# Performance work log

Hardware: AMD Instinct MI355X
Metric: run time of the kernel (lower is better)

## Reference

```python
import jax, jax.numpy as jnp
import numpy as np

NUM_REL = 6
EMBED_DIM = 128
B, N = 8, 1024


def _relation_type(dx, dy):
    # Faithful to _get_relation_type's if/elif chain (order matters).
    return jnp.select(
        [dy > 0.5,
         dy < -0.5,
         dx < -0.5,
         dx > 0.5,
         (jnp.abs(dx) < 0.3) & (jnp.abs(dy) < 0.3)],
        [0, 1, 2, 3, 4],
        5,
    )


def setup_inputs() -> dict:
    key = jax.random.key(0)
    k1, k2, k3, k4 = jax.random.split(key, 4)
    symbols = jax.random.normal(k1, (B, N, EMBED_DIM), dtype=jnp.float32)
    positions = jax.random.normal(k2, (B, N, 2), dtype=jnp.float32)
    # 6 Linear(embed_dim, embed_dim) layers, stacked: W [6, D, D] (torch layout: y = x @ W.T + b)
    bound = 1.0 / np.sqrt(EMBED_DIM)
    W = jax.random.uniform(k3, (NUM_REL, EMBED_DIM, EMBED_DIM), dtype=jnp.float32,
                           minval=-bound, maxval=bound)
    b = jax.random.uniform(k4, (NUM_REL, EMBED_DIM), dtype=jnp.float32,
                           minval=-bound, maxval=bound)
    return {"symbols": symbols, "positions": positions, "W": W, "b": b}


def reference(symbols, positions, W, b):
    Bn, Nn, D = symbols.shape
    # dx[b,i,j] = pos[b,j,0] - pos[b,i,0]; dy likewise (source i -> target j)
    dx = positions[:, None, :, 0] - positions[:, :, None, 0]  # [B, i, j]
    dy = positions[:, None, :, 1] - positions[:, :, None, 1]
    rel = _relation_type(dx, dy)  # [B, i, j] in {0..5}

    # Per-type transform of every source symbol: T[r,b,i,:] = symbols[b,i] @ W[r].T + b[r]
    T = jnp.einsum('bid,red->rbie', symbols, W) + b[:, None, None, :]  # [6, B, N, D]

    # One-hot relation mask with i != j excluded; scatter-add into targets j.
    not_diag = ~jnp.eye(Nn, dtype=bool)  # [i, j]
    mask = (rel[None] == jnp.arange(NUM_REL)[:, None, None, None]) & not_diag  # [6, B, i, j]
    agg = jnp.einsum('rbij,rbie->bje', mask.astype(symbols.dtype), T)  # [B, N, D]
    return symbols + agg
```

## Files before the change

### kernel.cpp

```cpp
#include <hip/hip_runtime.h>
#include <stdint.h>


typedef __attribute__((ext_vector_type(8))) short bf16x8;
typedef __attribute__((ext_vector_type(4))) float f32x4;
union U4B { uint4 u; bf16x8 b; };

#if defined(__has_builtin)
#  if __has_builtin(__builtin_amdgcn_global_load_lds)
#    define HAVE_GLL 1
#  endif
#  if __has_builtin(__builtin_amdgcn_mul_u24)
#    define OH_MUL24 1
#  endif
#endif

__device__ __forceinline__ uint16_t f2bf(float f) {
    union { float f; uint32_t u; } v; v.f = f;
    uint32_t u = v.u;
    uint32_t r = (u + 0x7FFFu + ((u >> 16) & 1u)) >> 16;
    return (uint16_t)r;
}

#define BARRIER_LGKM() do {                                   \
    asm volatile("s_waitcnt lgkmcnt(0)" ::: "memory");        \
    __builtin_amdgcn_s_barrier();                             \
    asm volatile("" ::: "memory");                            \
} while (0)

__global__ __launch_bounds__(256)
void prep_kernel(const float* __restrict__ X, const float* __restrict__ W,
                 uint16_t* __restrict__ symT, uint16_t* __restrict__ WtB,
                 float* __restrict__ T4) {
    const int blk = blockIdx.x, tid = threadIdx.x;
    if (blk < 256) {
        __shared__ float T[64 * 65];
        const int b = blk & 7, z = blk >> 3, it = z & 15, et = z >> 4;
        const int i0 = it * 64, e0 = et * 64;
        const float4* Xf = (const float4*)X;
#pragma unroll
        for (int s = 0; s < 4; ++s) {
            int il = s * 16 + (tid >> 4), e4 = tid & 15;
            float4 v = Xf[((size_t)b << 15) + (size_t)((i0 + il) << 5) + (e0 >> 2) + e4];
            T[il * 65 + e4 * 4 + 0] = v.x;
            T[il * 65 + e4 * 4 + 1] = v.y;
            T[il * 65 + e4 * 4 + 2] = v.z;
            T[il * 65 + e4 * 4 + 3] = v.w;
        }
        __syncthreads();
#pragma unroll
        for (int s = 0; s < 4; ++s) {
            int el = s * 16 + (tid >> 4), il4 = tid & 15;
            uint16_t h0 = f2bf(T[(il4 * 4 + 0) * 65 + el]);
            uint16_t h1 = f2bf(T[(il4 * 4 + 1) * 65 + el]);
            uint16_t h2 = f2bf(T[(il4 * 4 + 2) * 65 + el]);
            uint16_t h3 = f2bf(T[(il4 * 4 + 3) * 65 + el]);
            uint2 pk = { (uint32_t)h0 | ((uint32_t)h1 << 16),
                         (uint32_t)h2 | ((uint32_t)h3 << 16) };
            *(uint2*)&symT[((size_t)b << 17) + ((size_t)(e0 + el) << 10) + i0 + il4 * 4] = pk;
        }
    } else if (blk < 352) {
        int g = (blk - 256) * 256 + tid;
        float4 v = ((const float4*)W)[g];
        int r = g >> 12, rem = g & 4095, ep = rem >> 5, e4 = rem & 31;
        int kb = r * 4 + (e4 >> 3);
        int kc = (e4 & 7) * 4;
        uint16_t h0 = f2bf(v.x), h1 = f2bf(v.y), h2 = f2bf(v.z), h3 = f2bf(v.w);
        uint2 pk = { (uint32_t)h0 | ((uint32_t)h1 << 16),
                     (uint32_t)h2 | ((uint32_t)h3 << 16) };
        *(uint2*)&WtB[((size_t)(kb * 128 + ep)) * 32 + kc] = pk;
    } else {
        const int z = blk - 352, bb = z >> 2, qq = z & 3;
        const int e = tid & 127, half = tid >> 7;
        const float* base = X + (((size_t)(bb << 10) + (qq << 8) + (half << 7)) << 7) + e;
        float s = 0.f;
#pragma unroll 8
        for (int itr = 0; itr < 128; ++itr) s += base[(size_t)itr << 7];
        __shared__ float red[256];
        red[tid] = s;
        __syncthreads();
        if (tid < 128) T4[(z << 7) + tid] = red[tid] + red[tid + 128];
    }
}

#define SP 776

__global__ __launch_bounds__(512, 8)
void fused_kernel(const float* __restrict__ X, const float* __restrict__ pos,
                  const uint16_t* __restrict__ symT, const uint16_t* __restrict__ WtB,
                  const float* __restrict__ bias, const float* __restrict__ T4,
                  float* __restrict__ out) {
    __shared__ __align__(16) char smem[40960];
    float2*   posS  = (float2*)(smem + 16384);
    uint16_t* SA    = (uint16_t*)smem;
    float*    cntL  = (float*)(smem + 24832);
    uint32_t* rel32 = (uint32_t*)(smem + 32768);

    const int blk = blockIdx.x;
    const int b = blk & 7, jt = blk >> 3, j0 = jt * 8;
    const int tid = threadIdx.x;
    const int w = tid >> 6, lane = tid & 63, m = lane & 15, q = lane >> 4;

    const uint16_t* symTb = symT + ((size_t)b << 17);

    int goff[2];
#pragma unroll
    for (int s = 0; s < 2; ++s) {
        int e = (w << 4) + (s << 3) + (lane >> 3);
        int t = lane & 7;
        goff[s] = (e << 10) + ((t ^ (e & 7)) << 3);
    }

    auto issue_chunk = [&](int cidx, int bufsel) {
#ifdef HAVE_GLL
#pragma unroll
        for (int s = 0; s < 2; ++s) {
            const uint16_t* gp = symTb + goff[s] + cidx * 64;
            char* lp = smem + bufsel * 16384 + (w << 11) + (s << 10);
            typedef const __attribute__((address_space(1))) uint32_t gu32;
            typedef __attribute__((address_space(3))) uint32_t lu32;
            __builtin_amdgcn_global_load_lds((gu32*)gp, (lu32*)lp, 16, 0, 0);
        }
#else
#pragma unroll
        for (int s = 0; s < 2; ++s) {
            uint4 v = *(const uint4*)(symTb + goff[s] + cidx * 64);
            *(uint4*)(smem + bufsel * 16384 + (w << 11) + (s << 10) + lane * 16) = v;
        }
#endif
    };

    issue_chunk(0, 0);
    const float2* pos2 = (const float2*)pos + ((size_t)b << 10);
    float2 p0 = pos2[tid], p1 = pos2[tid + 512];
    posS[tid] = p0;
    posS[tid + 512] = p1;
    BARRIER_LGKM();

    {
        const int mm = tid & 7, grp = tid >> 3;
        const int j = j0 + mm;
        const float2 pj = posS[j];
        uint32_t* dst = &rel32[mm * 256];
        const int sw = mm * 2;
#pragma unroll
        for (int s = 0; s < 4; ++s) {
            uint32_t word = 0;
#pragma unroll
            for (int qq = 0; qq < 4; ++qq) {
                int i = grp * 16 + s * 4 + qq;
                float2 pi = posS[i];
                float dx = pj.x - pi.x, dy = pj.y - pi.y;
                int r = (dy > 0.5f) ? 0
                      : (dy < -0.5f) ? 1
                      : (dx < -0.5f) ? 2
                      : (dx > 0.5f)  ? 3
                      : (fabsf(dx) < 0.3f && fabsf(dy) < 0.3f) ? 4
                      : 5;
                uint32_t oh = (i == j) ? 0u : (1u << r);
                word |= oh << (8 * qq);
            }
            dst[(grp * 4 + s) ^ sw] = word;
        }
    }
    BARRIER_LGKM();

    f32x4 acc[5];
#pragma unroll
    for (int r = 0; r < 5; ++r) acc[r] = (f32x4){0.f, 0.f, 0.f, 0.f};

    const int E = (w << 4) + m;
    const int bseg0 = q ^ (m & 7);
    const int bseg1 = (4 + q) ^ (m & 7);
    const int m8 = m & 7;
    const int csw = m8 << 1;

    for (int c = 0; c < 16; ++c) {
        if (c < 15) {
            issue_chunk(c + 1, (c + 1) & 1);
            asm volatile("s_waitcnt vmcnt(2)" ::: "memory");
        } else {
            asm volatile("s_waitcnt vmcnt(0)" ::: "memory");
        }
        const char* bufc = smem + (c & 1) * 16384 + (w << 11) + (m << 7);
#pragma unroll
        for (int ks = 0; ks < 2; ++ks) {
            U4B bfr;
            bfr.u = *(const uint4*)(bufc + ((ks ? bseg1 : bseg0) << 4));
            uint2 cw = *(const uint2*)&rel32[m8 * 256 +
                           (((c << 4) + (ks << 3) + (q << 1)) ^ csw)];
            uint32_t hx01 = __builtin_amdgcn_perm(cw.x, cw.x, 0x01010000u) & 0x00FF00FFu;
            uint32_t hx23 = __builtin_amdgcn_perm(cw.x, cw.x, 0x03030202u) & 0x00FF00FFu;
            uint32_t hy01 = __builtin_amdgcn_perm(cw.y, cw.y, 0x01010000u) & 0x00FF00FFu;
            uint32_t hy23 = __builtin_amdgcn_perm(cw.y, cw.y, 0x03030202u) & 0x00FF00FFu;
#pragma unroll
            for (int r = 0; r < 5; ++r) {
                const uint32_t rm = 0x00010001u << r;
                U4B a;
#ifdef OH_MUL24
                const uint32_t mc = 0x3F80u >> r;
                a.u.x = (uint32_t)__builtin_amdgcn_mul_u24((int)(hx01 & rm), (int)mc);
                a.u.y = (uint32_t)__builtin_amdgcn_mul_u24((int)(hx23 & rm), (int)mc);
                a.u.z = (uint32_t)__builtin_amdgcn_mul_u24((int)(hy01 & rm), (int)mc);
                a.u.w = (uint32_t)__builtin_amdgcn_mul_u24((int)(hy23 & rm), (int)mc);
#else
                uint32_t g2;
                g2 = hx01 & rm; a.u.x = (g2 << (14 - r)) - (g2 << (7 - r));
                g2 = hx23 & rm; a.u.y = (g2 << (14 - r)) - (g2 << (7 - r));
                g2 = hy01 & rm; a.u.z = (g2 << (14 - r)) - (g2 << (7 - r));
                g2 = hy23 & rm; a.u.w = (g2 << (14 - r)) - (g2 << (7 - r));
#endif
                acc[r] = __builtin_amdgcn_mfma_f32_16x16x32_bf16(a.b, bfr.b, acc[r], 0, 0, 0);
            }
        }
    }
    BARRIER_LGKM();

    {
        const int j = tid >> 6, t = tid & 63;
        const uint32_t* row = &rel32[j * 256 + t * 4];
        uint32_t s0 = 0, s1 = 0, s2 = 0, s3 = 0, s4 = 0;
#pragma unroll
        for (int k = 0; k < 4; ++k) {
            uint32_t wd = row[k];
            s0 += wd & 0x01010101u;        s1 += (wd >> 1) & 0x01010101u;
            s2 += (wd >> 2) & 0x01010101u; s3 += (wd >> 3) & 0x01010101u;
            s4 += (wd >> 4) & 0x01010101u;
        }
        int cnt[6];
        cnt[0] = (int)((s0 * 0x01010101u) >> 24);
        cnt[1] = (int)((s1 * 0x01010101u) >> 24);
        cnt[2] = (int)((s2 * 0x01010101u) >> 24);
        cnt[3] = (int)((s3 * 0x01010101u) >> 24);
        cnt[4] = (int)((s4 * 0x01010101u) >> 24);
#pragma unroll
        for (int off = 1; off < 64; off <<= 1)
#pragma unroll
            for (int r = 0; r < 5; ++r)
                cnt[r] += __shfl_xor(cnt[r], off, 64);
        if (t == 0) {
#pragma unroll
            for (int r = 0; r < 5; ++r) cntL[j * 6 + r] = (float)cnt[r];
            cntL[j * 6 + 5] = (float)(1023 - cnt[0] - cnt[1] - cnt[2] - cnt[3] - cnt[4]);
        }
    }

#pragma unroll
    for (int r = 0; r < 5; ++r)
#pragma unroll
        for (int reg = 0; reg < 4; ++reg)
            SA[(q * 4 + reg) * SP + r * 128 + E] = f2bf(acc[r][reg]);
    {
        float ts = T4[((b << 2) + 0) * 128 + E] + T4[((b << 2) + 1) * 128 + E]
                 + T4[((b << 2) + 2) * 128 + E] + T4[((b << 2) + 3) * 128 + E];
#pragma unroll
        for (int reg = 0; reg < 4; ++reg) {
            float symj = X[((size_t)((b << 10) + j0 + (((q << 2) + reg) & 7)) << 7) + E];
            float s5 = ts - symj
                     - acc[0][reg] - acc[1][reg] - acc[2][reg] - acc[3][reg] - acc[4][reg];
            SA[(q * 4 + reg) * SP + 5 * 128 + E] = f2bf(s5);
        }
    }
    BARRIER_LGKM();

    {
        f32x4 c3 = (f32x4){0.f, 0.f, 0.f, 0.f};
#pragma unroll
        for (int kb = 0; kb < 24; ++kb) {
            U4B af, bw;
            af.u = *(const uint4*)&SA[m * SP + kb * 32 + q * 8];
            bw.u = *(const uint4*)&WtB[((size_t)(kb * 128 + (w << 4) + m)) * 32 + q * 8];
            c3 = __builtin_amdgcn_mfma_f32_16x16x32_bf16(af.b, bw.b, c3, 0, 0, 0);
        }

        const int e = (w << 4) + m;
        float be[6];
#pragma unroll
        for (int r = 0; r < 6; ++r) be[r] = bias[r * 128 + e];
#pragma unroll
        for (int reg = 0; reg < 4; ++reg) {
            const int j = q * 4 + reg;
            if (j < 8) {
                float add = c3[reg];
#pragma unroll
                for (int r = 0; r < 6; ++r) add += cntL[j * 6 + r] * be[r];
                size_t o = ((size_t)((b << 10) + j0 + j) << 7) + e;
                out[o] = X[o] + add;
            }
        }
    }
}

extern "C" void kernel_launch(void* const* d_in, const int* in_sizes, int n_in,
                              void* d_out, int out_size, void* d_ws, size_t ws_size,
                              hipStream_t stream) {
    const float* symbols   = (const float*)d_in[0];
    const float* positions = (const float*)d_in[1];
    const float* W         = (const float*)d_in[2];
    const float* bias      = (const float*)d_in[3];
    float* out             = (float*)d_out;

    char* ws = (char*)d_ws;
    uint16_t* symT = (uint16_t*)ws;
    uint16_t* WtB  = (uint16_t*)(ws + 2097152);
    float*    T4   = (float*)(ws + 2097152 + 196608);

    prep_kernel<<<384, 256, 0, stream>>>(symbols, W, symT, WtB, T4);
    fused_kernel<<<1024, 512, 0, stream>>>(symbols, positions, symT, WtB, bias, T4, out);
}
```

Before: 111.7 us.

## Split source dimension in halves with 16 targets per block and reduce partials

Each block now handles 16 target rows over half of the source rows instead of 8 targets over all sources, so the 16-row MFMA tile is fully used rather than half wasted. Both halves write partial results to a workspace buffer, and a new elementwise kernel sums the two partials with the residual input. This makes each streamed symbol chunk serve twice as many targets, cutting symT traffic, but it adds an extra launch and a 2x4MB partial write and read.

```diff
diff --git a/kernel.cpp b/kernel.cpp
--- a/kernel.cpp
+++ b/kernel.cpp
@@ -86,10 +86,10 @@
 #define SP 776
 
 __global__ __launch_bounds__(512, 8)
-void fused_kernel(const float* __restrict__ X, const float* __restrict__ pos,
-                  const uint16_t* __restrict__ symT, const uint16_t* __restrict__ WtB,
-                  const float* __restrict__ bias, const float* __restrict__ T4,
-                  float* __restrict__ out) {
+void fused_a(const float* __restrict__ X, const float* __restrict__ pos,
+             const uint16_t* __restrict__ symT, const uint16_t* __restrict__ WtB,
+             const float* __restrict__ bias, const float* __restrict__ T4,
+             float* __restrict__ parts) {
     __shared__ __align__(16) char smem[40960];
     float2*   posS  = (float2*)(smem + 16384);
     uint16_t* SA    = (uint16_t*)smem;
@@ -97,11 +97,12 @@
     uint32_t* rel32 = (uint32_t*)(smem + 32768);
 
     const int blk = blockIdx.x;
-    const int b = blk & 7, jt = blk >> 3, j0 = jt * 8;
+    const int b = blk & 7, z = blk >> 3, jt = z >> 1, h = z & 1;
+    const int j0 = jt * 16;
     const int tid = threadIdx.x;
     const int w = tid >> 6, lane = tid & 63, m = lane & 15, q = lane >> 4;
 
-    const uint16_t* symTb = symT + ((size_t)b << 17);
+    const uint16_t* symTbh = symT + ((size_t)b << 17) + (h << 9);
 
     int goff[2];
 #pragma unroll
@@ -115,7 +116,7 @@
 #ifdef HAVE_GLL
 #pragma unroll
         for (int s = 0; s < 2; ++s) {
-            const uint16_t* gp = symTb + goff[s] + cidx * 64;
+            const uint16_t* gp = symTbh + goff[s] + cidx * 64;
             char* lp = smem + bufsel * 16384 + (w << 11) + (s << 10);
             typedef const __attribute__((address_space(1))) uint32_t gu32;
             typedef __attribute__((address_space(3))) uint32_t lu32;
@@ -124,7 +125,7 @@
 #else
 #pragma unroll
         for (int s = 0; s < 2; ++s) {
-            uint4 v = *(const uint4*)(symTb + goff[s] + cidx * 64);
+            uint4 v = *(const uint4*)(symTbh + goff[s] + cidx * 64);
             *(uint4*)(smem + bufsel * 16384 + (w << 11) + (s << 10) + lane * 16) = v;
         }
 #endif
@@ -138,17 +139,17 @@
     BARRIER_LGKM();
 
     {
-        const int mm = tid & 7, grp = tid >> 3;
+        const int mm = tid & 15, grp = tid >> 4;
         const int j = j0 + mm;
         const float2 pj = posS[j];
-        uint32_t* dst = &rel32[mm * 256];
+        uint32_t* dst = &rel32[mm * 128];
         const int sw = mm * 2;
 #pragma unroll
         for (int s = 0; s < 4; ++s) {
             uint32_t word = 0;
 #pragma unroll
             for (int qq = 0; qq < 4; ++qq) {
-                int i = grp * 16 + s * 4 + qq;
+                int i = (h << 9) + grp * 16 + s * 4 + qq;
                 float2 pi = posS[i];
                 float dx = pj.x - pi.x, dy = pj.y - pi.y;
                 int r = (dy > 0.5f) ? 0
@@ -172,11 +173,10 @@
     const int E = (w << 4) + m;
     const int bseg0 = q ^ (m & 7);
     const int bseg1 = (4 + q) ^ (m & 7);
-    const int m8 = m & 7;
-    const int csw = m8 << 1;
-
-    for (int c = 0; c < 16; ++c) {
-        if (c < 15) {
+    const int csw = m << 1;
+
+    for (int c = 0; c < 8; ++c) {
+        if (c < 7) {
             issue_chunk(c + 1, (c + 1) & 1);
             asm volatile("s_waitcnt vmcnt(2)" ::: "memory");
         } else {
@@ -187,7 +187,7 @@
         for (int ks = 0; ks < 2; ++ks) {
             U4B bfr;
             bfr.u = *(const uint4*)(bufc + ((ks ? bseg1 : bseg0) << 4));
-            uint2 cw = *(const uint2*)&rel32[m8 * 256 +
+            uint2 cw = *(const uint2*)&rel32[m * 128 +
                            (((c << 4) + (ks << 3) + (q << 1)) ^ csw)];
             uint32_t hx01 = __builtin_amdgcn_perm(cw.x, cw.x, 0x01010000u) & 0x00FF00FFu;
             uint32_t hx23 = __builtin_amdgcn_perm(cw.x, cw.x, 0x03030202u) & 0x00FF00FFu;
@@ -216,9 +216,10 @@
     }
     BARRIER_LGKM();
 
+    const int diag = ((jt >> 5) == h) ? 1 : 0;
     {
-        const int j = tid >> 6, t = tid & 63;
-        const uint32_t* row = &rel32[j * 256 + t * 4];
+        const int j = tid >> 5, t = tid & 31;
+        const uint32_t* row = &rel32[j * 128 + t * 4];
         uint32_t s0 = 0, s1 = 0, s2 = 0, s3 = 0, s4 = 0;
 #pragma unroll
         for (int k = 0; k < 4; ++k) {
@@ -234,14 +235,14 @@
         cnt[3] = (int)((s3 * 0x01010101u) >> 24);
         cnt[4] = (int)((s4 * 0x01010101u) >> 24);
 #pragma unroll
-        for (int off = 1; off < 64; off <<= 1)
+        for (int off = 1; off < 32; off <<= 1)
 #pragma unroll
             for (int r = 0; r < 5; ++r)
                 cnt[r] += __shfl_xor(cnt[r], off, 64);
         if (t == 0) {
 #pragma unroll
             for (int r = 0; r < 5; ++r) cntL[j * 6 + r] = (float)cnt[r];
-            cntL[j * 6 + 5] = (float)(1023 - cnt[0] - cnt[1] - cnt[2] - cnt[3] - cnt[4]);
+            cntL[j * 6 + 5] = (float)(512 - diag - cnt[0] - cnt[1] - cnt[2] - cnt[3] - cnt[4]);
         }
     }
 
@@ -251,14 +252,15 @@
         for (int reg = 0; reg < 4; ++reg)
             SA[(q * 4 + reg) * SP + r * 128 + E] = f2bf(acc[r][reg]);
     {
-        float ts = T4[((b << 2) + 0) * 128 + E] + T4[((b << 2) + 1) * 128 + E]
-                 + T4[((b << 2) + 2) * 128 + E] + T4[((b << 2) + 3) * 128 + E];
+        float ts = T4[(((b << 2) + (h << 1)) << 7) + E]
+                 + T4[(((b << 2) + (h << 1) + 1) << 7) + E];
 #pragma unroll
         for (int reg = 0; reg < 4; ++reg) {
-            float symj = X[((size_t)((b << 10) + j0 + (((q << 2) + reg) & 7)) << 7) + E];
+            const int j = (q << 2) + reg;
+            float symj = diag ? X[((size_t)((b << 10) + j0 + j) << 7) + E] : 0.f;
             float s5 = ts - symj
                      - acc[0][reg] - acc[1][reg] - acc[2][reg] - acc[3][reg] - acc[4][reg];
-            SA[(q * 4 + reg) * SP + 5 * 128 + E] = f2bf(s5);
+            SA[j * SP + 5 * 128 + E] = f2bf(s5);
         }
     }
     BARRIER_LGKM();
@@ -277,18 +279,29 @@
         float be[6];
 #pragma unroll
         for (int r = 0; r < 6; ++r) be[r] = bias[r * 128 + e];
+        float* part = parts + ((size_t)h << 20);
 #pragma unroll
         for (int reg = 0; reg < 4; ++reg) {
             const int j = q * 4 + reg;
-            if (j < 8) {
-                float add = c3[reg];
-#pragma unroll
-                for (int r = 0; r < 6; ++r) add += cntL[j * 6 + r] * be[r];
-                size_t o = ((size_t)((b << 10) + j0 + j) << 7) + e;
-                out[o] = X[o] + add;
-            }
-        }
-    }
+            float add = c3[reg];
+#pragma unroll
+            for (int r = 0; r < 6; ++r) add += cntL[j * 6 + r] * be[r];
+            part[((size_t)((b << 10) + j0 + j) << 7) + e] = add;
+        }
+    }
+}
+
+__global__ __launch_bounds__(256)
+void fused_b(const float* __restrict__ X, const float* __restrict__ parts,
+             float* __restrict__ out) {
+    const int g = blockIdx.x * 256 + threadIdx.x;
+    const float4* X4 = (const float4*)X;
+    const float4* P0 = (const float4*)parts;
+    const float4* P1 = (const float4*)(parts + (1u << 20));
+    float4 x = X4[g], a = P0[g], c = P1[g];
+    float4 o = { x.x + a.x + c.x, x.y + a.y + c.y,
+                 x.z + a.z + c.z, x.w + a.w + c.w };
+    ((float4*)out)[g] = o;
 }
 
 extern "C" void kernel_launch(void* const* d_in, const int* in_sizes, int n_in,
@@ -304,7 +317,9 @@
     uint16_t* symT = (uint16_t*)ws;
     uint16_t* WtB  = (uint16_t*)(ws + 2097152);
     float*    T4   = (float*)(ws + 2097152 + 196608);
+    float*    part = (float*)(ws + 2310144);
 
     prep_kernel<<<384, 256, 0, stream>>>(symbols, W, symT, WtB, T4);
-    fused_kernel<<<1024, 512, 0, stream>>>(symbols, positions, symT, WtB, bias, T4, out);
-}
+    fused_a<<<1024, 512, 0, stream>>>(symbols, positions, symT, WtB, bias, T4, part);
+    fused_b<<<1024, 256, 0, stream>>>(symbols, part, out);
+}
```

Measured after the change: 105.9 us. 5.2% less time.
